# Performance work log

Measured on AMD Instinct MI355X. Metric: run time of the kernel, lower is better.

## Reference

```python
import jax, jax.numpy as jnp
import numpy as np

CONV_KERNEL_MAX_DIFF = 0.7  # self.conv_kernel_max_diff
PRE_KERNEL_MULT = 1.0       # self.pre_conv_kernel_mult


def setup_inputs() -> dict:
    B, C, N, K = 8, 64, 32, 3
    key = jax.random.key(0)
    k1, k2, k3 = jax.random.split(key, 3)
    conv_in = jax.random.normal(k1, (B, C, N, N), dtype=jnp.float32)
    pre_kernel = jax.random.normal(k2, (B, C, C, K, K), dtype=jnp.float32)
    bias = jax.random.normal(k3, (B, C, 1, 1), dtype=jnp.float32)
    return {"conv_in": conv_in, "pre_kernel": pre_kernel, "bias": bias}


def _identity_kernel(c, k, dtype):
    # 1 at the spatial center for matching in/out channel -> identity circular conv
    idx = jnp.arange(c)
    return jnp.zeros((c, c, k, k), dtype=dtype).at[idx, idx, k // 2, k // 2].set(1.0)


def reference(conv_in, pre_kernel, bias):
    B, C, N, _ = conv_in.shape
    Kk = pre_kernel.shape[-1]
    # K = 0.7 * tanh(pre_kernel) + I
    Kmat = CONV_KERNEL_MAX_DIFF * jnp.tanh(PRE_KERNEL_MULT * pre_kernel)
    Kmat = Kmat + _identity_kernel(C, Kk, conv_in.dtype)[None]
    # Embed k x k kernel into n x n with the center tap at the origin
    # (so the identity kernel acts as the identity map under circular conv).
    Kpad = jnp.zeros((B, C, C, N, N), dtype=conv_in.dtype).at[..., :Kk, :Kk].set(Kmat)
    Kpad = jnp.roll(Kpad, shift=(-(Kk // 2), -(Kk // 2)), axis=(-2, -1))
    # Circular conv2D diagonalizes per-frequency into c x c complex matrices.
    K_hat = jnp.fft.fft2(Kpad)            # [B,C,C,N,N] complex
    x_hat = jnp.fft.fft2(conv_in)         # [B,C,N,N] complex
    y_hat = jnp.einsum('boiuv,biuv->bouv', K_hat, x_hat)
    conv_out = jnp.real(jnp.fft.ifft2(y_hat)) + bias
    # log|det| of the block-circulant operator = sum over frequencies of
    # log|det K_hat[:, :, u, v]| (Schur-complement recursion in the original).
    mats = jnp.transpose(K_hat, (0, 3, 4, 1, 2))  # [B,N,N,C,C]
    _, logabsdet = jnp.linalg.slogdet(mats)
    logdet = jnp.sum(logabsdet, axis=(1, 2))      # [B]
    return conv_out, logdet
```

## Files before the change

### kernel.cpp

```cpp
#include <hip/hip_runtime.h>
#include <math.h>

#define BB 8
#define CC 64
#define NN 32
#define CONV_TOTAL (BB*CC*NN*NN)
#define KM_ELEMS (BB*9*CC*CC)
#define NCANON 514

typedef float v2f __attribute__((ext_vector_type(2)));

#define RL(x, l) __uint_as_float(__builtin_amdgcn_readlane(__float_as_uint(x), (l)))

#define SW(r, c) ((((r) << 6)) | ((c) ^ (r)))

__global__ __launch_bounds__(256) void build_km(const float* __restrict__ pre,
                                                float* __restrict__ km,
                                                float* __restrict__ logdet_out) {
    int idx = blockIdx.x * 256 + threadIdx.x;
    if (blockIdx.x == 0 && threadIdx.x < BB) logdet_out[threadIdx.x] = 0.f;
    if (idx >= KM_ELEMS) return;
    int b   = idx / (9 * 4096);
    int rem = idx - b * (9 * 4096);
    int j   = rem >> 12;
    int e   = rem & 4095;
    int o = e >> 6, i = e & 63;
    float v = 0.7f * tanhf(pre[(b * 4096 + e) * 9 + j]);
    if (o == i && j == 4) v += 1.0f;
    km[idx] = v;
}

__global__ __launch_bounds__(256) void conv_kernel(const float* __restrict__ x,
                                                   const float* __restrict__ km,
                                                   const float* __restrict__ bias,
                                                   float* __restrict__ out) {
    int b = blockIdx.x >> 6, o = blockIdx.x & 63;
    __shared__ float Kms[9][64];
    __shared__ float xs[1024];
    int t = threadIdx.x;
    for (int s = t; s < 576; s += 256) {
        int j = s >> 6, i = s & 63;
        Kms[j][i] = km[(b * 9 + j) * 4096 + (o << 6) + i];
    }
    float bb = bias[(b << 6) + o];
    float acc0 = bb, acc1 = bb, acc2 = bb, acc3 = bb;
    int u = t >> 3, v0 = (t & 7) << 2;
    const float* xb = x + (size_t)(b << 6) * 1024;
    for (int i = 0; i < 64; ++i) {
        float4 xv4 = *(const float4*)(xb + i * 1024 + (t << 2));
        __syncthreads();
        *(float4*)&xs[t << 2] = xv4;
        __syncthreads();
        #pragma unroll
        for (int dy = 0; dy < 3; ++dy) {
            int row = (u + 1 - dy) & 31;
            const float* xr = &xs[row << 5];
            float xv[6];
            #pragma unroll
            for (int q = 0; q < 6; ++q) xv[q] = xr[(v0 - 1 + q) & 31];
            #pragma unroll
            for (int dx = 0; dx < 3; ++dx) {
                float w = Kms[dy * 3 + dx][i];
                acc0 += w * xv[2 - dx];
                acc1 += w * xv[3 - dx];
                acc2 += w * xv[4 - dx];
                acc3 += w * xv[5 - dx];
            }
        }
    }
    float4 r = make_float4(acc0, acc1, acc2, acc3);
    *(float4*)(out + ((size_t)blockIdx.x << 10) + (u << 5) + v0) = r;
}

__global__ __launch_bounds__(256, 3) void logdet_kernel(const float* __restrict__ km,
                                                        float* __restrict__ logdet_out) {
    int gid = blockIdx.x;
    int b = gid / NCANON, ci = gid - b * NCANON;
    int u, v;
    if (ci < 17)        { u = 0;                  v = ci; }
    else if (ci < 497)  { int r = ci - 17; u = 1 + (r >> 5); v = r & 31; }
    else                { u = 16;                 v = ci - 497; }
    float wgt = ((u == 0 || u == 16) && (v == 0 || v == 16)) ? 1.0f : 2.0f;

    int t = threadIdx.x;
    int wave = t >> 6, lane = t & 63;

    __shared__ v2f As[4096];

    float wr[9], wi[9];
    #pragma unroll
    for (int j = 0; j < 9; ++j) {
        int dy = j / 3, dx = j % 3;
        float argrev = -(float)(u * (dy - 1) + v * (dx - 1)) * (1.0f / 32.0f);
        argrev = argrev - floorf(argrev);
        wr[j] = __builtin_amdgcn_cosf(argrev);
        wi[j] = __builtin_amdgcn_sinf(argrev);
    }

    const float* Kb = km + (size_t)b * 36864;
    #pragma unroll
    for (int rep = 0; rep < 16; ++rep) {
        int e = t + (rep << 8);
        int r = e >> 6, c = e & 63;
        float re = 0.f, im = 0.f;
        #pragma unroll
        for (int j = 0; j < 9; ++j) {
            float kv = Kb[(j << 12) + e];
            re = fmaf(kv, wr[j], re);
            im = fmaf(kv, wi[j], im);
        }
        As[SW(r, c)] = (v2f){re, im};
    }
    __syncthreads();

    float lsum = 0.f;
    for (int p = 0; p < 8; ++p) {
        int K0 = p << 3, K7 = K0 | 7;
        if (wave == 0) {
            int r = lane;
            v2f pc[8];
            #pragma unroll
            for (int j = 0; j < 8; ++j) pc[j] = As[SW(r, K0 + j)];
            #pragma unroll
            for (int k = 0; k < 8; ++k) {
                int K = K0 + k;
                float px = RL(pc[k].x, K), py = RL(pc[k].y, K);
                float mag = fmaf(px, px, py * py);
                lsum += 0.5f * __logf(mag);
                float inv = __builtin_amdgcn_rcpf(mag);
                float mr = (pc[k].x * px + pc[k].y * py) * inv;
                float mi = (pc[k].y * px - pc[k].x * py) * inv;
                bool act = r > K;
                mr = act ? mr : 0.f;
                mi = act ? mi : 0.f;
                pc[k].x = act ? mr : pc[k].x;
                pc[k].y = act ? mi : pc[k].y;
                #pragma unroll
                for (int j = k + 1; j < 8; ++j) {
                    float ux = RL(pc[j].x, K), uy = RL(pc[j].y, K);
                    pc[j].x = fmaf(-mr, ux, fmaf( mi, uy, pc[j].x));
                    pc[j].y = fmaf(-mr, uy, fmaf(-mi, ux, pc[j].y));
                }
            }
            #pragma unroll
            for (int j = 0; j < 8; ++j) As[SW(r, K0 + j)] = pc[j];

            if (p < 7) {
                int c = lane;
                v2f uu[8];
                #pragma unroll
                for (int j = 0; j < 8; ++j) uu[j] = As[SW(K0 + j, c)];
                #pragma unroll
                for (int j = 1; j < 8; ++j) {
                    #pragma unroll
                    for (int j2 = 0; j2 < 8; ++j2) {
                        if (j2 >= j) continue;
                        v2f L = As[SW(K0 + j, K0 + j2)];
                        uu[j].x = fmaf(-L.x, uu[j2].x, fmaf( L.y, uu[j2].y, uu[j].x));
                        uu[j].y = fmaf(-L.x, uu[j2].y, fmaf(-L.y, uu[j2].x, uu[j].y));
                    }
                }
                if (c > K7) {
                    #pragma unroll
                    for (int j = 0; j < 8; ++j) As[SW(K0 + j, c)] = uu[j];
                }
            }
        }
        __syncthreads();
        if (p < 7) {
            int r = lane;
            bool actr = r > K7;
            v2f l1[8], l2[8];
            #pragma unroll
            for (int j = 0; j < 8; ++j) {
                v2f L = As[SW(r, K0 + j)];
                float lx = actr ? L.x : 0.f;
                float ly = actr ? L.y : 0.f;
                l1[j] = (v2f){-lx, -lx};
                l2[j] = (v2f){ ly, -ly};
            }
            for (int i = 0; i < 16; ++i) {
                int c = (i << 2) | wave;
                if (c > K7) {
                    v2f a = As[SW(r, c)];
                    #pragma unroll
                    for (int j = 0; j < 8; ++j) {
                        v2f U = As[SW(K0 + j, c)];
                        v2f u2 = (v2f){U.y, U.x};
                        a = l1[j] * U  + a;
                        a = l2[j] * u2 + a;
                    }
                    As[SW(r, c)] = a;
                }
            }
        }
        __syncthreads();
    }
    if (t == 0) atomicAdd(&logdet_out[b], wgt * lsum);
}

extern "C" void kernel_launch(void* const* d_in, const int* in_sizes, int n_in,
                              void* d_out, int out_size, void* d_ws, size_t ws_size,
                              hipStream_t stream) {
    const float* conv_in    = (const float*)d_in[0];
    const float* pre_kernel = (const float*)d_in[1];
    const float* bias       = (const float*)d_in[2];
    float* out = (float*)d_out;
    float* km  = (float*)d_ws;
    float* logdet_out = out + CONV_TOTAL;

    build_km<<<KM_ELEMS / 256, 256, 0, stream>>>(pre_kernel, km, logdet_out);
    conv_kernel<<<BB * CC, 256, 0, stream>>>(conv_in, km, bias, out);
    logdet_kernel<<<BB * NCANON, 256, 0, stream>>>(km, logdet_out);
}
```

Measured before the change: 231.0 us.

## Restructure blocked LU logdet using L-inverse and packed float4 column pairs

```diff
diff --git a/kernel.cpp b/kernel.cpp
--- a/kernel.cpp
+++ b/kernel.cpp
@@ -12,7 +12,7 @@
 
 #define RL(x, l) __uint_as_float(__builtin_amdgcn_readlane(__float_as_uint(x), (l)))
 
-#define SW(r, c) ((((r) << 6)) | ((c) ^ (r)))
+#define PIDX(r, cp) (((r) << 5) | ((cp) ^ ((r) & 31)))
 
 __global__ __launch_bounds__(256) void build_km(const float* __restrict__ pre,
                                                 float* __restrict__ km,
@@ -85,7 +85,8 @@
     int t = threadIdx.x;
     int wave = t >> 6, lane = t & 63;
 
-    __shared__ v2f As[4096];
+    __shared__ float4 As[2048];
+    __shared__ v2f LinvS[8][8];
 
     float wr[9], wi[9];
     #pragma unroll
@@ -99,28 +100,34 @@
 
     const float* Kb = km + (size_t)b * 36864;
     #pragma unroll
-    for (int rep = 0; rep < 16; ++rep) {
-        int e = t + (rep << 8);
-        int r = e >> 6, c = e & 63;
-        float re = 0.f, im = 0.f;
+    for (int rep = 0; rep < 8; ++rep) {
+        int e2 = t + (rep << 8);
+        int r = e2 >> 5, cp = e2 & 31;
+        int e = e2 << 1;
+        float re0 = 0.f, im0 = 0.f, re1 = 0.f, im1 = 0.f;
         #pragma unroll
         for (int j = 0; j < 9; ++j) {
-            float kv = Kb[(j << 12) + e];
-            re = fmaf(kv, wr[j], re);
-            im = fmaf(kv, wi[j], im);
-        }
-        As[SW(r, c)] = (v2f){re, im};
+            float2 kv = *(const float2*)(Kb + (j << 12) + e);
+            re0 = fmaf(kv.x, wr[j], re0); im0 = fmaf(kv.x, wi[j], im0);
+            re1 = fmaf(kv.y, wr[j], re1); im1 = fmaf(kv.y, wi[j], im1);
+        }
+        As[PIDX(r, cp)] = make_float4(re0, im0, re1, im1);
     }
     __syncthreads();
 
     float lsum = 0.f;
     for (int p = 0; p < 8; ++p) {
         int K0 = p << 3, K7 = K0 | 7;
+        int pb = p << 2;
         if (wave == 0) {
             int r = lane;
             v2f pc[8];
             #pragma unroll
-            for (int j = 0; j < 8; ++j) pc[j] = As[SW(r, K0 + j)];
+            for (int q = 0; q < 4; ++q) {
+                float4 f = As[PIDX(r, pb + q)];
+                pc[2*q]   = (v2f){f.x, f.y};
+                pc[2*q+1] = (v2f){f.z, f.w};
+            }
             #pragma unroll
             for (int k = 0; k < 8; ++k) {
                 int K = K0 + k;
@@ -131,8 +138,7 @@
                 float mr = (pc[k].x * px + pc[k].y * py) * inv;
                 float mi = (pc[k].y * px - pc[k].x * py) * inv;
                 bool act = r > K;
-                mr = act ? mr : 0.f;
-                mi = act ? mi : 0.f;
+                mr = act ? mr : 0.f; mi = act ? mi : 0.f;
                 pc[k].x = act ? mr : pc[k].x;
                 pc[k].y = act ? mi : pc[k].y;
                 #pragma unroll
@@ -143,55 +149,80 @@
                 }
             }
             #pragma unroll
-            for (int j = 0; j < 8; ++j) As[SW(r, K0 + j)] = pc[j];
+            for (int q = 0; q < 4; ++q)
+                As[PIDX(r, pb + q)] =
+                    make_float4(pc[2*q].x, pc[2*q].y, pc[2*q+1].x, pc[2*q+1].y);
 
             if (p < 7) {
-                int c = lane;
-                v2f uu[8];
-                #pragma unroll
-                for (int j = 0; j < 8; ++j) uu[j] = As[SW(K0 + j, c)];
+                v2f x[8];
+                #pragma unroll
+                for (int j = 0; j < 8; ++j)
+                    x[j] = (v2f){(lane == j) ? 1.f : 0.f, 0.f};
                 #pragma unroll
                 for (int j = 1; j < 8; ++j) {
                     #pragma unroll
-                    for (int j2 = 0; j2 < 8; ++j2) {
-                        if (j2 >= j) continue;
-                        v2f L = As[SW(K0 + j, K0 + j2)];
-                        uu[j].x = fmaf(-L.x, uu[j2].x, fmaf( L.y, uu[j2].y, uu[j].x));
-                        uu[j].y = fmaf(-L.x, uu[j2].y, fmaf(-L.y, uu[j2].x, uu[j].y));
+                    for (int tq = 0; tq < j; ++tq) {
+                        float ljx = RL(pc[tq].x, K0 + j);
+                        float ljy = RL(pc[tq].y, K0 + j);
+                        x[j].x = fmaf(-ljx, x[tq].x, fmaf( ljy, x[tq].y, x[j].x));
+                        x[j].y = fmaf(-ljx, x[tq].y, fmaf(-ljy, x[tq].x, x[j].y));
                     }
                 }
-                if (c > K7) {
+                if (lane < 8) {
                     #pragma unroll
-                    for (int j = 0; j < 8; ++j) As[SW(K0 + j, c)] = uu[j];
+                    for (int j = 0; j < 8; ++j) LinvS[j][lane] = x[j];
                 }
             }
         }
         __syncthreads();
         if (p < 7) {
             int r = lane;
+            v2f l8[8];
+            #pragma unroll
+            for (int q = 0; q < 4; ++q) {
+                float4 f = As[PIDX(r, pb + q)];
+                l8[2*q]   = (v2f){f.x, f.y};
+                l8[2*q+1] = (v2f){f.z, f.w};
+            }
+            v2f W0 = (v2f){0.f, 0.f}, W1 = (v2f){0.f, 0.f};
+            #pragma unroll
+            for (int tq = 0; tq < 8; ++tq) {
+                v2f Lt = l8[tq];
+                v2f i0 = LinvS[tq][2*wave];
+                v2f i1 = LinvS[tq][2*wave + 1];
+                W0.x = fmaf(Lt.x, i0.x, fmaf(-Lt.y, i0.y, W0.x));
+                W0.y = fmaf(Lt.x, i0.y, fmaf( Lt.y, i0.x, W0.y));
+                W1.x = fmaf(Lt.x, i1.x, fmaf(-Lt.y, i1.y, W1.x));
+                W1.y = fmaf(Lt.x, i1.y, fmaf( Lt.y, i1.x, W1.y));
+            }
+            __syncthreads();
+            if (r > K7)
+                As[PIDX(r, pb + wave)] = make_float4(W0.x, W0.y, W1.x, W1.y);
+            __syncthreads();
+
+            v2f wn1[8], wn2[8];
             bool actr = r > K7;
-            v2f l1[8], l2[8];
-            #pragma unroll
-            for (int j = 0; j < 8; ++j) {
-                v2f L = As[SW(r, K0 + j)];
-                float lx = actr ? L.x : 0.f;
-                float ly = actr ? L.y : 0.f;
-                l1[j] = (v2f){-lx, -lx};
-                l2[j] = (v2f){ ly, -ly};
-            }
-            for (int i = 0; i < 16; ++i) {
-                int c = (i << 2) | wave;
-                if (c > K7) {
-                    v2f a = As[SW(r, c)];
-                    #pragma unroll
-                    for (int j = 0; j < 8; ++j) {
-                        v2f U = As[SW(K0 + j, c)];
-                        v2f u2 = (v2f){U.y, U.x};
-                        a = l1[j] * U  + a;
-                        a = l2[j] * u2 + a;
-                    }
-                    As[SW(r, c)] = a;
-                }
+            #pragma unroll
+            for (int q = 0; q < 4; ++q) {
+                float4 f = As[PIDX(r, pb + q)];
+                float w0x = actr ? f.x : 0.f, w0y = actr ? f.y : 0.f;
+                float w1x = actr ? f.z : 0.f, w1y = actr ? f.w : 0.f;
+                wn1[2*q]   = (v2f){-w0x, -w0x};  wn2[2*q]   = (v2f){ w0y, -w0y};
+                wn1[2*q+1] = (v2f){-w1x, -w1x};  wn2[2*q+1] = (v2f){ w1y, -w1y};
+            }
+            for (int cp = pb + 4 + wave; cp < 32; cp += 4) {
+                float4 a = As[PIDX(r, cp)];
+                v2f a0 = (v2f){a.x, a.y}, a1 = (v2f){a.z, a.w};
+                #pragma unroll
+                for (int j = 0; j < 8; ++j) {
+                    float4 Tp = As[PIDX(K0 + j, cp)];
+                    v2f T0 = (v2f){Tp.x, Tp.y}, T1 = (v2f){Tp.z, Tp.w};
+                    a0 = wn1[j] * T0 + a0;
+                    a0 = wn2[j] * (v2f){T0.y, T0.x} + a0;
+                    a1 = wn1[j] * T1 + a1;
+                    a1 = wn2[j] * (v2f){T1.y, T1.x} + a1;
+                }
+                if (actr) As[PIDX(r, cp)] = make_float4(a0.x, a0.y, a1.x, a1.y);
             }
         }
         __syncthreads();
```

Result: no change. 230.2 us (-0.4%).

## Transpose logdet matrix to column-major and fold panel solve into redundant per-wave factorization

Applied to the files above, without the earlier changes.

```diff
diff --git a/kernel.cpp b/kernel.cpp
--- a/kernel.cpp
+++ b/kernel.cpp
@@ -11,8 +11,6 @@
 typedef float v2f __attribute__((ext_vector_type(2)));
 
 #define RL(x, l) __uint_as_float(__builtin_amdgcn_readlane(__float_as_uint(x), (l)))
-
-#define SW(r, c) ((((r) << 6)) | ((c) ^ (r)))
 
 __global__ __launch_bounds__(256) void build_km(const float* __restrict__ pre,
                                                 float* __restrict__ km,
@@ -24,8 +22,8 @@
     int rem = idx - b * (9 * 4096);
     int j   = rem >> 12;
     int e   = rem & 4095;
-    int o = e >> 6, i = e & 63;
-    float v = 0.7f * tanhf(pre[(b * 4096 + e) * 9 + j]);
+    int o = e & 63, i = e >> 6;
+    float v = 0.7f * tanhf(pre[(b * 4096 + o * 64 + i) * 9 + j]);
     if (o == i && j == 4) v += 1.0f;
     km[idx] = v;
 }
@@ -40,7 +38,7 @@
     int t = threadIdx.x;
     for (int s = t; s < 576; s += 256) {
         int j = s >> 6, i = s & 63;
-        Kms[j][i] = km[(b * 9 + j) * 4096 + (o << 6) + i];
+        Kms[j][i] = km[(b * 9 + j) * 4096 + (i << 6) + o];
     }
     float bb = bias[(b << 6) + o];
     float acc0 = bb, acc1 = bb, acc2 = bb, acc3 = bb;
@@ -72,8 +70,8 @@
     *(float4*)(out + ((size_t)blockIdx.x << 10) + (u << 5) + v0) = r;
 }
 
-__global__ __launch_bounds__(256, 3) void logdet_kernel(const float* __restrict__ km,
-                                                        float* __restrict__ logdet_out) {
+__global__ __launch_bounds__(256) void logdet_kernel(const float* __restrict__ km,
+                                                     float* __restrict__ logdet_out) {
     int gid = blockIdx.x;
     int b = gid / NCANON, ci = gid - b * NCANON;
     int u, v;
@@ -99,99 +97,88 @@
 
     const float* Kb = km + (size_t)b * 36864;
     #pragma unroll
-    for (int rep = 0; rep < 16; ++rep) {
-        int e = t + (rep << 8);
-        int r = e >> 6, c = e & 63;
-        float re = 0.f, im = 0.f;
+    for (int rep = 0; rep < 8; ++rep) {
+        int e2 = t + (rep << 8);
+        float re0 = 0.f, im0 = 0.f, re1 = 0.f, im1 = 0.f;
         #pragma unroll
         for (int j = 0; j < 9; ++j) {
-            float kv = Kb[(j << 12) + e];
-            re = fmaf(kv, wr[j], re);
-            im = fmaf(kv, wi[j], im);
-        }
-        As[SW(r, c)] = (v2f){re, im};
+            float2 kv = *(const float2*)(Kb + (j << 12) + (e2 << 1));
+            re0 = fmaf(kv.x, wr[j], re0); im0 = fmaf(kv.x, wi[j], im0);
+            re1 = fmaf(kv.y, wr[j], re1); im1 = fmaf(kv.y, wi[j], im1);
+        }
+        *(float4*)&As[e2 << 1] = make_float4(re0, im0, re1, im1);
     }
     __syncthreads();
 
     float lsum = 0.f;
+    int r = lane;
     for (int p = 0; p < 8; ++p) {
         int K0 = p << 3, K7 = K0 | 7;
-        if (wave == 0) {
-            int r = lane;
-            v2f pc[8];
-            #pragma unroll
-            for (int j = 0; j < 8; ++j) pc[j] = As[SW(r, K0 + j)];
-            #pragma unroll
-            for (int k = 0; k < 8; ++k) {
-                int K = K0 + k;
-                float px = RL(pc[k].x, K), py = RL(pc[k].y, K);
-                float mag = fmaf(px, px, py * py);
-                lsum += 0.5f * __logf(mag);
-                float inv = __builtin_amdgcn_rcpf(mag);
-                float mr = (pc[k].x * px + pc[k].y * py) * inv;
-                float mi = (pc[k].y * px - pc[k].x * py) * inv;
-                bool act = r > K;
-                mr = act ? mr : 0.f;
-                mi = act ? mi : 0.f;
-                pc[k].x = act ? mr : pc[k].x;
-                pc[k].y = act ? mi : pc[k].y;
+
+        v2f pc[8];
+        #pragma unroll
+        for (int j = 0; j < 8; ++j) pc[j] = As[((K0 + j) << 6) | r];
+        #pragma unroll
+        for (int k = 0; k < 8; ++k) {
+            int K = K0 + k;
+            float px = RL(pc[k].x, K), py = RL(pc[k].y, K);
+            float mag = fmaf(px, px, py * py);
+            lsum += 0.5f * __logf(mag);
+            float inv = __builtin_amdgcn_rcpf(mag);
+            float mr = (pc[k].x * px + pc[k].y * py) * inv;
+            float mi = (pc[k].y * px - pc[k].x * py) * inv;
+            bool act = r > K;
+            mr = act ? mr : 0.f; mi = act ? mi : 0.f;
+            pc[k].x = act ? mr : pc[k].x;
+            pc[k].y = act ? mi : pc[k].y;
+            #pragma unroll
+            for (int j = k + 1; j < 8; ++j) {
+                float ux = RL(pc[j].x, K), uy = RL(pc[j].y, K);
+                pc[j].x = fmaf(-mr, ux, fmaf( mi, uy, pc[j].x));
+                pc[j].y = fmaf(-mr, uy, fmaf(-mi, ux, pc[j].y));
+            }
+        }
+
+        if (p < 7) {
+            bool act = r > K7;
+            v2f W[8];
+            #pragma unroll
+            for (int j = 7; j >= 0; --j) {
+                v2f w = pc[j];
                 #pragma unroll
-                for (int j = k + 1; j < 8; ++j) {
-                    float ux = RL(pc[j].x, K), uy = RL(pc[j].y, K);
-                    pc[j].x = fmaf(-mr, ux, fmaf( mi, uy, pc[j].x));
-                    pc[j].y = fmaf(-mr, uy, fmaf(-mi, ux, pc[j].y));
+                for (int q = j + 1; q < 8; ++q) {
+                    float lx = RL(pc[j].x, K0 + q), ly = RL(pc[j].y, K0 + q);
+                    w.x = fmaf(-W[q].x, lx, fmaf( W[q].y, ly, w.x));
+                    w.y = fmaf(-W[q].x, ly, fmaf(-W[q].y, lx, w.y));
                 }
-            }
-            #pragma unroll
-            for (int j = 0; j < 8; ++j) As[SW(r, K0 + j)] = pc[j];
-
-            if (p < 7) {
-                int c = lane;
-                v2f uu[8];
-                #pragma unroll
-                for (int j = 0; j < 8; ++j) uu[j] = As[SW(K0 + j, c)];
-                #pragma unroll
-                for (int j = 1; j < 8; ++j) {
-                    #pragma unroll
-                    for (int j2 = 0; j2 < 8; ++j2) {
-                        if (j2 >= j) continue;
-                        v2f L = As[SW(K0 + j, K0 + j2)];
-                        uu[j].x = fmaf(-L.x, uu[j2].x, fmaf( L.y, uu[j2].y, uu[j].x));
-                        uu[j].y = fmaf(-L.x, uu[j2].y, fmaf(-L.y, uu[j2].x, uu[j].y));
-                    }
-                }
-                if (c > K7) {
-                    #pragma unroll
-                    for (int j = 0; j < 8; ++j) As[SW(K0 + j, c)] = uu[j];
-                }
-            }
-        }
-        __syncthreads();
-        if (p < 7) {
-            int r = lane;
-            bool actr = r > K7;
-            v2f l1[8], l2[8];
-            #pragma unroll
-            for (int j = 0; j < 8; ++j) {
-                v2f L = As[SW(r, K0 + j)];
-                float lx = actr ? L.x : 0.f;
-                float ly = actr ? L.y : 0.f;
-                l1[j] = (v2f){-lx, -lx};
-                l2[j] = (v2f){ ly, -ly};
-            }
-            for (int i = 0; i < 16; ++i) {
-                int c = (i << 2) | wave;
-                if (c > K7) {
-                    v2f a = As[SW(r, c)];
-                    #pragma unroll
-                    for (int j = 0; j < 8; ++j) {
-                        v2f U = As[SW(K0 + j, c)];
-                        v2f u2 = (v2f){U.y, U.x};
-                        a = l1[j] * U  + a;
-                        a = l2[j] * u2 + a;
-                    }
-                    As[SW(r, c)] = a;
-                }
+                W[j].x = act ? w.x : 0.f;
+                W[j].y = act ? w.y : 0.f;
+            }
+
+            for (int c = K0 + 8 + wave; c < 64; c += 4) {
+                v2f* col = As + (c << 6);
+                v2f a = col[r];
+                float4 t01 = *(const float4*)(col + K0);
+                float4 t23 = *(const float4*)(col + K0 + 2);
+                float4 t45 = *(const float4*)(col + K0 + 4);
+                float4 t67 = *(const float4*)(col + K0 + 6);
+                a.x = fmaf(-W[0].x, t01.x, fmaf( W[0].y, t01.y, a.x));
+                a.y = fmaf(-W[0].x, t01.y, fmaf(-W[0].y, t01.x, a.y));
+                a.x = fmaf(-W[1].x, t01.z, fmaf( W[1].y, t01.w, a.x));
+                a.y = fmaf(-W[1].x, t01.w, fmaf(-W[1].y, t01.z, a.y));
+                a.x = fmaf(-W[2].x, t23.x, fmaf( W[2].y, t23.y, a.x));
+                a.y = fmaf(-W[2].x, t23.y, fmaf(-W[2].y, t23.x, a.y));
+                a.x = fmaf(-W[3].x, t23.z, fmaf( W[3].y, t23.w, a.x));
+                a.y = fmaf(-W[3].x, t23.w, fmaf(-W[3].y, t23.z, a.y));
+                a.x = fmaf(-W[4].x, t45.x, fmaf( W[4].y, t45.y, a.x));
+                a.y = fmaf(-W[4].x, t45.y, fmaf(-W[4].y, t45.x, a.y));
+                a.x = fmaf(-W[5].x, t45.z, fmaf( W[5].y, t45.w, a.x));
+                a.y = fmaf(-W[5].x, t45.w, fmaf(-W[5].y, t45.z, a.y));
+                a.x = fmaf(-W[6].x, t67.x, fmaf( W[6].y, t67.y, a.x));
+                a.y = fmaf(-W[6].x, t67.y, fmaf(-W[6].y, t67.x, a.y));
+                a.x = fmaf(-W[7].x, t67.z, fmaf( W[7].y, t67.w, a.x));
+                a.y = fmaf(-W[7].x, t67.w, fmaf(-W[7].y, t67.z, a.y));
+                if (act) col[r] = a;
             }
         }
         __syncthreads();
```

Result: slower. 269.2 us (+16.5%).
